# Optimization experiments

Measured on AMD Instinct MI355X. Metric: run time of the kernel, lower is better.

## Reference

```python
import jax, jax.numpy as jnp
import numpy as np

T, B, H = 512, 32, 512   # seq, batch, hidden_dim (hidden has 2*H channels)
D = 512                  # label_dim
V = 32000                # vocab
L = 2048                 # number of labels (spans)
K = 2                    # tags per label (regularized ragged tags)


def setup_inputs() -> dict:
    key = jax.random.key(0)
    ks = jax.random.split(key, 11)
    hidden = jax.random.normal(ks[0], (T, B, 2 * H), dtype=jnp.float32)
    begins = jax.random.randint(ks[1], (L,), 1, T - 1)   # begin-1 >= 0
    ends = jax.random.randint(ks[2], (L,), 1, T - 1)     # end <= T-1, end-1 >= 0
    bids = jax.random.randint(ks[3], (L,), 0, B)
    tags = jax.random.randint(ks[4], (L, K), 0, V)
    s = 1.0 / np.sqrt(2 * H)
    Wc = jax.random.uniform(ks[5], (D, 2 * H), minval=-s, maxval=s, dtype=jnp.float32)
    bc = jax.random.uniform(ks[6], (D,), minval=-s, maxval=s, dtype=jnp.float32)
    Wp = jax.random.uniform(ks[7], (D, 2 * H), minval=-s, maxval=s, dtype=jnp.float32)
    bp = jax.random.uniform(ks[8], (D,), minval=-s, maxval=s, dtype=jnp.float32)
    s2 = 1.0 / np.sqrt(D)
    Wo = jax.random.uniform(ks[9], (V, D), minval=-s2, maxval=s2, dtype=jnp.float32)
    bo = jnp.zeros((V,), jnp.float32)
    # discard probs per SoftmaxLoss._discard_probs from synthetic counts
    counts = jax.random.uniform(ks[10], (V,), minval=0.5, maxval=100.0, dtype=jnp.float32)
    freqs = counts / counts.sum()
    discard_probs = jnp.maximum(1.0 - jnp.sqrt(1e-4 / freqs), 0.0)
    return dict(hidden=hidden, Wc=Wc, bc=bc, Wp=Wp, bp=bp, Wo=Wo, bo=bo,
                discard_probs=discard_probs, begins=begins, ends=ends,
                bids=bids, tags=tags)


def reference(hidden, Wc, bc, Wp, bp, Wo, bo, discard_probs,
              begins, ends, bids, tags):
    Hd = hidden.shape[-1] // 2
    # span gathers (vectorized over all labels)
    h_bm1 = hidden[begins - 1, bids]                 # [L, 2H]
    h_end = hidden[ends, bids]                       # [L, 2H]
    context = jnp.concatenate([h_bm1[:, :Hd], h_end[:, Hd:]], axis=-1)  # [L, 2H]
    phrase = (hidden[begins, bids] + hidden[ends - 1, bids]) * 0.5      # [L, 2H]
    # FFNs (dropout = identity in eval mode)
    cf = jnp.tanh(context @ Wc.T + bc)               # [L, D]
    pf = jnp.tanh(phrase @ Wp.T + bp)                # [L, D]
    feats = jnp.concatenate([cf, pf], axis=0)        # [2L, D]
    # softmax loss with discard-prob scaling
    logsm = jax.nn.log_softmax(feats @ Wo.T + bo, axis=-1)  # [2L, V]
    tg = jnp.concatenate([tags, tags], axis=0)       # [2L, K]
    neg = -jnp.take_along_axis(logsm, tg, axis=-1)   # [2L, K]
    ratio = 1.0 - discard_probs[tg]                  # [2L, K]
    loss_rows = (neg * ratio).sum(-1) / ratio.sum(-1)  # [2L]
    n = tg.shape[0]
    return (loss_rows.sum() / (n + 1e-5)).reshape(1)
```

## Files before the change

### kernel.cpp

```cpp
#include <hip/hip_runtime.h>
#include <stdint.h>

typedef uint16_t u16;
typedef uint8_t  u8;
typedef __bf16 bf16x8 __attribute__((ext_vector_type(8)));
typedef float f32x4 __attribute__((ext_vector_type(4)));
typedef int i32x4 __attribute__((ext_vector_type(4)));
typedef int i32x8 __attribute__((ext_vector_type(8)));

#define NSC    16
#define NTILES 250
#define NPART  (2 * NSC)
#define NROWS  4096

__device__ __forceinline__ u16 f2b(float x) {
    uint32_t u = __float_as_uint(x);
    u += 0x7FFF + ((u >> 16) & 1);
    return (u16)(u >> 16);
}

__device__ __forceinline__ u8 f32_to_fp8(float x) {
    uint32_t sign = (__float_as_uint(x) >> 24) & 0x80;
    float ax = fminf(fabsf(x), 448.f);
    uint32_t r;
    if (ax < 0.015625f) {
        r = (uint32_t)(int)rintf(ax * 512.f);
    } else {
        uint32_t u = __float_as_uint(ax);
        u += 0x0007FFFF + ((u >> 20) & 1);
        r = (((u >> 23) - 120) << 3) | ((u >> 20) & 7);
    }
    return (u8)(sign | r);
}

__device__ __forceinline__ float fp8_val(int b) {
    int e = (b >> 3) & 0xF, m = b & 7;
    float v = e ? __uint_as_float((uint32_t)(((e + 120) << 23) | (m << 20)))
                : (float)m * 0.001953125f;
    return (b & 0x80) ? -v : v;
}

__device__ __forceinline__ void cp16(const void* g, void* l) {
    __builtin_amdgcn_global_load_lds(
        (const __attribute__((address_space(1))) uint32_t*)g,
        (__attribute__((address_space(3))) uint32_t*)l, 16, 0, 0);
}

__device__ __forceinline__ float fast_tanh(float x) {
    x = fminf(15.f, fmaxf(-15.f, x));
    float e = __expf(2.f * x);
    return (e - 1.f) / (e + 1.f);
}

__global__ void k_convert8(const float* __restrict__ src, u8* __restrict__ dst, int n) {
    int i = (blockIdx.x * blockDim.x + threadIdx.x) * 4;
    int stride = gridDim.x * blockDim.x * 4;
    for (; i < n; i += stride) {
        float4 v = *(const float4*)(src + i);
        u8 o[4] = {f32_to_fp8(v.x * 32.f), f32_to_fp8(v.y * 32.f),
                   f32_to_fp8(v.z * 32.f), f32_to_fp8(v.w * 32.f)};
        *(uint32_t*)(dst + i) = *(const uint32_t*)o;
    }
}

__global__ void k_prep(const float* __restrict__ Wc, const float* __restrict__ Wp,
                       const float* __restrict__ hidden, const int* __restrict__ begins,
                       const int* __restrict__ ends, const int* __restrict__ bids,
                       u16* __restrict__ Wc_b, u16* __restrict__ Wp_b,
                       u16* __restrict__ ctx, u16* __restrict__ phr) {
    int b = blockIdx.x;
    if (b < 256) {
        int i = b * 2048 + threadIdx.x * 8;
        float4 a0 = *(const float4*)(Wc + i), a1 = *(const float4*)(Wc + i + 4);
        float4 p0 = *(const float4*)(Wp + i), p1 = *(const float4*)(Wp + i + 4);
        u16 oc[8] = {f2b(a0.x), f2b(a0.y), f2b(a0.z), f2b(a0.w),
                     f2b(a1.x), f2b(a1.y), f2b(a1.z), f2b(a1.w)};
        u16 op[8] = {f2b(p0.x), f2b(p0.y), f2b(p0.z), f2b(p0.w),
                     f2b(p1.x), f2b(p1.y), f2b(p1.z), f2b(p1.w)};
        *(int4*)(Wc_b + i) = *(const int4*)oc;
        *(int4*)(Wp_b + i) = *(const int4*)op;
        return;
    }
    int l = b - 256;
    int bg = begins[l], e = ends[l], bd = bids[l];
    const float* h_bm1 = hidden + ((size_t)(bg - 1) * 32 + bd) * 1024;
    const float* h_e   = hidden + ((size_t)e * 32 + bd) * 1024;
    const float* h_b   = hidden + ((size_t)bg * 32 + bd) * 1024;
    const float* h_em1 = hidden + ((size_t)(e - 1) * 32 + bd) * 1024;
    int d = threadIdx.x * 4;
    float4 c4 = (d < 512) ? *(const float4*)(h_bm1 + d) : *(const float4*)(h_e + d);
    float4 b4 = *(const float4*)(h_b + d);
    float4 e4 = *(const float4*)(h_em1 + d);
    u16 co[4] = {f2b(c4.x), f2b(c4.y), f2b(c4.z), f2b(c4.w)};
    u16 po[4] = {f2b(0.5f * (b4.x + e4.x)), f2b(0.5f * (b4.y + e4.y)),
                 f2b(0.5f * (b4.z + e4.z)), f2b(0.5f * (b4.w + e4.w))};
    *(uint64_t*)(ctx + (size_t)l * 1024 + d) = *(const uint64_t*)co;
    *(uint64_t*)(phr + (size_t)l * 1024 + d) = *(const uint64_t*)po;
}

__global__ __launch_bounds__(256) void k_feats(const u16* __restrict__ ctx, const u16* __restrict__ phr,
        const u16* __restrict__ Wc, const u16* __restrict__ Wp,
        const float* __restrict__ bc, const float* __restrict__ bp,
        u8* __restrict__ feats) {
    __shared__ __align__(16) u16 lA[64 * 32];
    __shared__ __align__(16) u16 lB[64 * 32];
    int z = blockIdx.z;
    const u16* A = z ? phr : ctx;
    const u16* W = z ? Wp : Wc;
    const float* bias = z ? bp : bc;
    int m0 = blockIdx.x * 64;
    int n0 = blockIdx.y * 64;
    int t = threadIdx.x;
    int lane = t & 63, w = t >> 6;
    int lrow = lane & 15, lq = lane >> 4;
    f32x4 zero = {0.f, 0.f, 0.f, 0.f};
    f32x4 acc[4];
    for (int i = 0; i < 4; i++) acc[i] = zero;
    int row = t >> 2, kseg = (t & 3) * 8;
    for (int kt = 0; kt < 32; kt++) {
        int k0 = kt * 32;
        __syncthreads();
        cp16(&A[(size_t)(m0 + row) * 1024 + k0 + kseg], &lA[t * 8]);
        cp16(&W[(size_t)(n0 + row) * 1024 + k0 + kseg], &lB[t * 8]);
        __syncthreads();
        bf16x8 af = *(bf16x8*)&lA[(w * 16 + lrow) * 32 + lq * 8];
        for (int ns = 0; ns < 4; ns++) {
            bf16x8 bfr = *(bf16x8*)&lB[(ns * 16 + lrow) * 32 + lq * 8];
            acc[ns] = __builtin_amdgcn_mfma_f32_16x16x32_bf16(af, bfr, acc[ns], 0, 0, 0);
        }
    }
    int zbase = z * 2048;
    for (int ns = 0; ns < 4; ns++) {
        int col = n0 + ns * 16 + lrow;
        float bv = bias[col];
        for (int r = 0; r < 4; r++) {
            int orow = zbase + m0 + w * 16 + lq * 4 + r;
            feats[(size_t)orow * 512 + col] = f32_to_fp8(16.f * fast_tanh(acc[ns][r] + bv));
        }
    }
}

__global__ __launch_bounds__(256) void k_lse(const u8* __restrict__ feats,
        const u8* __restrict__ Wo, const float* __restrict__ bo, float* __restrict__ ps) {
    __shared__ __align__(16) u8 lds[2][2][128 * 128];
    int m0 = blockIdx.x * 128;
    int sc = blockIdx.y;
    int ts = (NTILES * sc) / NSC, te = (NTILES * (sc + 1)) / NSC;
    int t = threadIdx.x;
    int lane = t & 63, w = t >> 6;
    int lrow = lane & 15, lq = lane >> 4;
    int wrow = (w & 1) * 64, wcol = (w >> 1) * 64;
    int xm = lrow & 7;
    int xoA = ((2 * lq) ^ xm) * 16;
    int xoB = ((2 * lq + 1) ^ xm) * 16;

    int srow = t >> 3;
    int kb = ((t & 7) ^ ((t >> 3) & 7)) * 16;
    const u8* pA = feats + (size_t)(m0 + srow) * 512 + kb;

    int rowA[4], rowB[4];
    for (int i = 0; i < 4; i++) {
        rowA[i] = (wrow + i * 16 + lrow) * 128;
        rowB[i] = (wcol + i * 16 + lrow) * 128;
    }

    float s_state[4][4];
    for (int mi = 0; mi < 4; mi++)
        for (int r = 0; r < 4; r++) s_state[mi][r] = 0.f;
    f32x4 zero = {0.f, 0.f, 0.f, 0.f};
    f32x4 acc[4][4];
    const float inv512 = 1.f / 512.f;

    auto stage = [&](int buf, int gr) {
        int k0 = (gr & 3) * 128;
        const u8* pB = Wo + (size_t)((gr >> 2) * 128 + srow) * 512 + kb;
        const u8* pA2 = pA + k0;
        for (int j = 0; j < 4; j++) {
            cp16(pA2 + (size_t)(32 * j) * 512, &lds[buf][0][t * 16 + j * 4096]);
            cp16(pB + k0 + (size_t)(32 * j) * 512, &lds[buf][1][t * 16 + j * 4096]);
        }
    };

    int gr0 = ts * 4, gr1 = te * 4;
    stage(0, gr0);
    for (int gr = gr0; gr < gr1; gr++) {
        int cur = gr & 1;
        __syncthreads();
        if (gr + 1 < gr1) stage(cur ^ 1, gr + 1);
        if ((gr & 3) == 0)
            for (int mi = 0; mi < 4; mi++)
                for (int ni = 0; ni < 4; ni++) acc[mi][ni] = zero;
        const u8* bufA = lds[cur][0];
        const u8* bufB = lds[cur][1];
        i32x8 af[4];
        for (int mi = 0; mi < 4; mi++) {
            i32x4 lo = *(const i32x4*)(bufA + rowA[mi] + xoA);
            i32x4 hi = *(const i32x4*)(bufA + rowA[mi] + xoB);
            af[mi] = __builtin_shufflevector(lo, hi, 0, 1, 2, 3, 4, 5, 6, 7);
        }
        for (int ni = 0; ni < 4; ni++) {
            i32x4 blo = *(const i32x4*)(bufB + rowB[ni] + xoA);
            i32x4 bhi = *(const i32x4*)(bufB + rowB[ni] + xoB);
            i32x8 bf8 = __builtin_shufflevector(blo, bhi, 0, 1, 2, 3, 4, 5, 6, 7);
            for (int mi = 0; mi < 4; mi++)
                acc[mi][ni] = __builtin_amdgcn_mfma_scale_f32_16x16x128_f8f6f4(
                    af[mi], bf8, acc[mi][ni], 0, 0,
                    0, 0x7F7F7F7F, 0, 0x7F7F7F7F);
        }
        if ((gr & 3) == 3) {
            int n0 = (gr >> 2) * 128;
            for (int ni = 0; ni < 4; ni++) {
                float bv = bo[n0 + wcol + ni * 16 + lrow];
                for (int mi = 0; mi < 4; mi++)
                    for (int r = 0; r < 4; r++)
                        s_state[mi][r] += __expf(fmaf(acc[mi][ni][r], inv512, bv));
            }
        }
    }
    for (int mi = 0; mi < 4; mi++)
    for (int r = 0; r < 4; r++) {
        float s = s_state[mi][r];
        for (int off = 1; off < 16; off <<= 1) s += __shfl_xor(s, off);
        if (lrow == 0) {
            int row = m0 + wrow + mi * 16 + lq * 4 + r;
            ps[row * NPART + sc * 2 + (w >> 1)] = s;
        }
    }
}

__global__ void k_taglog(const u8* __restrict__ feats, const u8* __restrict__ Wo,
        const float* __restrict__ bo, const int* __restrict__ tags, float* __restrict__ tlog) {
    int i = blockIdx.x * 4 + (threadIdx.x >> 6);
    int lane = threadIdx.x & 63;
    int t0 = tags[(i & 2047) * 2 + 0];
    int t1 = tags[(i & 2047) * 2 + 1];
    uint64_t fa = *(const uint64_t*)(feats + (size_t)i * 512 + lane * 8);
    uint64_t wa = *(const uint64_t*)(Wo + (size_t)t0 * 512 + lane * 8);
    uint64_t wb = *(const uint64_t*)(Wo + (size_t)t1 * 512 + lane * 8);
    float s0 = 0.f, s1 = 0.f;
    for (int j = 0; j < 8; j++) {
        float fv = fp8_val((int)((fa >> (8 * j)) & 0xFF));
        s0 += fv * fp8_val((int)((wa >> (8 * j)) & 0xFF));
        s1 += fv * fp8_val((int)((wb >> (8 * j)) & 0xFF));
    }
    for (int off = 32; off >= 1; off >>= 1) {
        s0 += __shfl_down(s0, off);
        s1 += __shfl_down(s1, off);
    }
    if (lane == 0) {
        tlog[i * 2 + 0] = s0 * (1.f / 512.f) + bo[t0];
        tlog[i * 2 + 1] = s1 * (1.f / 512.f) + bo[t1];
    }
}

__global__ void k_final(const float* __restrict__ ps,
        const float* __restrict__ tlog, const int* __restrict__ tags,
        const float* __restrict__ dp, float* __restrict__ out) {
    __shared__ float red[256];
    int i = blockIdx.x * 256 + threadIdx.x;
    float S = 0.f;
    for (int j = 0; j < NPART; j++) S += ps[i * NPART + j];
    float lse = logf(S);
    float num = 0.f, den = 0.f;
    for (int k = 0; k < 2; k++) {
        int tg = tags[(i & 2047) * 2 + k];
        float r = 1.0f - dp[tg];
        num += r * (lse - tlog[i * 2 + k]);
        den += r;
    }
    red[threadIdx.x] = num / den;
    __syncthreads();
    for (int s = 128; s > 0; s >>= 1) {
        if (threadIdx.x < s) red[threadIdx.x] += red[threadIdx.x + s];
        __syncthreads();
    }
    if (threadIdx.x == 0) atomicAdd(out, red[0] / (4096.0f + 1e-5f));
}

extern "C" void kernel_launch(void* const* d_in, const int* in_sizes, int n_in,
                              void* d_out, int out_size, void* d_ws, size_t ws_size,
                              hipStream_t stream) {
    const float* hidden = (const float*)d_in[0];
    const float* Wc     = (const float*)d_in[1];
    const float* bc     = (const float*)d_in[2];
    const float* Wp     = (const float*)d_in[3];
    const float* bp     = (const float*)d_in[4];
    const float* Wo     = (const float*)d_in[5];
    const float* bo     = (const float*)d_in[6];
    const float* dp     = (const float*)d_in[7];
    const int* begins   = (const int*)d_in[8];
    const int* ends     = (const int*)d_in[9];
    const int* bids     = (const int*)d_in[10];
    const int* tags     = (const int*)d_in[11];
    float* out = (float*)d_out;

    u8*  Wo8     = (u8*)d_ws;
    u16* Wc_b    = (u16*)((char*)d_ws + 16384000);
    u16* Wp_b    = Wc_b + 524288;
    u16* ctx_b   = Wp_b + 524288;
    u16* phr_b   = ctx_b + 2097152;
    u8*  feats8  = (u8*)(phr_b + 2097152);
    float* ps    = (float*)ctx_b;
    float* tlog  = ps + NROWS * NPART;

    k_convert8<<<2048, 256, 0, stream>>>(Wo, Wo8, 16384000);
    k_prep<<<2304, 256, 0, stream>>>(Wc, Wp, hidden, begins, ends, bids,
                                     Wc_b, Wp_b, ctx_b, phr_b);
    k_feats<<<dim3(32, 8, 2), 256, 0, stream>>>(ctx_b, phr_b, Wc_b, Wp_b, bc, bp, feats8);
    k_lse<<<dim3(32, NSC), 256, 0, stream>>>(feats8, Wo8, bo, ps);
    k_taglog<<<1024, 256, 0, stream>>>(feats8, Wo8, bo, tags, tlog);
    hipMemsetAsync(d_out, 0, sizeof(float), stream);
    k_final<<<16, 256, 0, stream>>>(ps, tlog, tags, dp, out);
}
```

Measured before the change: 280.0 us.

## Keep A fragments in registers and deepen B staging to four LDS slots

The LSE GEMM kernel now loads the whole 128x512 fp8 A block for each warp into registers once, so only Wo tiles are streamed through LDS. B staging moves from a double buffer to a four-slot ring with three tiles in flight, using explicit vmcnt waits and raw s_barrier in place of __syncthreads. It also raises MFMA issue priority and sets launch bounds for 2 blocks per CU. This halves LDS traffic and deepens prefetch, at the cost of many more VGPRs held for A fragments. It also relies on hand-counted waitcnt values being correct.

```diff
diff --git a/kernel.cpp b/kernel.cpp
--- a/kernel.cpp
+++ b/kernel.cpp
@@ -140,9 +140,9 @@
     }
 }
 
-__global__ __launch_bounds__(256) void k_lse(const u8* __restrict__ feats,
+__global__ __launch_bounds__(256, 2) void k_lse(const u8* __restrict__ feats,
         const u8* __restrict__ Wo, const float* __restrict__ bo, float* __restrict__ ps) {
-    __shared__ __align__(16) u8 lds[2][2][128 * 128];
+    __shared__ __align__(16) u8 lds[4][128 * 128];
     int m0 = blockIdx.x * 128;
     int sc = blockIdx.y;
     int ts = (NTILES * sc) / NSC, te = (NTILES * (sc + 1)) / NSC;
@@ -156,13 +156,24 @@
 
     int srow = t >> 3;
     int kb = ((t & 7) ^ ((t >> 3) & 7)) * 16;
-    const u8* pA = feats + (size_t)(m0 + srow) * 512 + kb;
-
-    int rowA[4], rowB[4];
-    for (int i = 0; i < 4; i++) {
-        rowA[i] = (wrow + i * 16 + lrow) * 128;
-        rowB[i] = (wcol + i * 16 + lrow) * 128;
-    }
+
+    i32x8 af[4][4];
+#pragma unroll
+    for (int mi = 0; mi < 4; mi++)
+#pragma unroll
+        for (int kc = 0; kc < 4; kc++) {
+            const u8* pa = feats + (size_t)(m0 + wrow + mi * 16 + lrow) * 512
+                         + kc * 128 + lq * 32;
+            i32x4 lo = *(const i32x4*)pa;
+            i32x4 hi = *(const i32x4*)(pa + 16);
+            af[mi][kc] = __builtin_shufflevector(lo, hi, 0, 1, 2, 3, 4, 5, 6, 7);
+        }
+
+    auto stageB = [&](int slot, int gr) {
+        const u8* pB = Wo + (size_t)((gr >> 2) * 128 + srow) * 512 + (gr & 3) * 128 + kb;
+        for (int j = 0; j < 4; j++)
+            cp16(pB + (size_t)(32 * j) * 512, &lds[slot][t * 16 + j * 4096]);
+    };
 
     float s_state[4][4];
     for (int mi = 0; mi < 4; mi++)
@@ -171,50 +182,54 @@
     f32x4 acc[4][4];
     const float inv512 = 1.f / 512.f;
 
-    auto stage = [&](int buf, int gr) {
-        int k0 = (gr & 3) * 128;
-        const u8* pB = Wo + (size_t)((gr >> 2) * 128 + srow) * 512 + kb;
-        const u8* pA2 = pA + k0;
-        for (int j = 0; j < 4; j++) {
-            cp16(pA2 + (size_t)(32 * j) * 512, &lds[buf][0][t * 16 + j * 4096]);
-            cp16(pB + k0 + (size_t)(32 * j) * 512, &lds[buf][1][t * 16 + j * 4096]);
-        }
-    };
-
-    int gr0 = ts * 4, gr1 = te * 4;
-    stage(0, gr0);
-    for (int gr = gr0; gr < gr1; gr++) {
-        int cur = gr & 1;
-        __syncthreads();
-        if (gr + 1 < gr1) stage(cur ^ 1, gr + 1);
-        if ((gr & 3) == 0)
+    int gr0 = ts * 4;
+    stageB(0, gr0);
+    stageB(1, gr0 + 1);
+    stageB(2, gr0 + 2);
+
+    for (int tile = ts; tile < te; ++tile) {
+        int grt = tile * 4;
+        bool notlast = (tile + 1 < te);
+#pragma unroll
+        for (int mi = 0; mi < 4; mi++)
+#pragma unroll
+            for (int ni = 0; ni < 4; ni++) acc[mi][ni] = zero;
+#pragma unroll
+        for (int kc = 0; kc < 4; kc++) {
+            if (notlast || kc < 2)
+                asm volatile("s_waitcnt vmcnt(8)" ::: "memory");
+            else if (kc == 2)
+                asm volatile("s_waitcnt vmcnt(4)" ::: "memory");
+            else
+                asm volatile("s_waitcnt vmcnt(0)" ::: "memory");
+            __builtin_amdgcn_s_barrier();
+            if (notlast || kc == 0)
+                stageB((kc + 3) & 3, grt + kc + 3);
+            const u8* bufB = lds[kc];
+            __builtin_amdgcn_s_setprio(1);
+#pragma unroll
+            for (int ni = 0; ni < 4; ni++) {
+                const u8* pb = bufB + (wcol + ni * 16 + lrow) * 128;
+                i32x4 blo = *(const i32x4*)(pb + xoA);
+                i32x4 bhi = *(const i32x4*)(pb + xoB);
+                i32x8 bfr = __builtin_shufflevector(blo, bhi, 0, 1, 2, 3, 4, 5, 6, 7);
+#pragma unroll
+                for (int mi = 0; mi < 4; mi++)
+                    acc[mi][ni] = __builtin_amdgcn_mfma_scale_f32_16x16x128_f8f6f4(
+                        af[mi][kc], bfr, acc[mi][ni], 0, 0,
+                        0, 0x7F7F7F7F, 0, 0x7F7F7F7F);
+            }
+            __builtin_amdgcn_s_setprio(0);
+        }
+        int n0 = tile * 128;
+#pragma unroll
+        for (int ni = 0; ni < 4; ni++) {
+            float bv = bo[n0 + wcol + ni * 16 + lrow];
+#pragma unroll
             for (int mi = 0; mi < 4; mi++)
-                for (int ni = 0; ni < 4; ni++) acc[mi][ni] = zero;
-        const u8* bufA = lds[cur][0];
-        const u8* bufB = lds[cur][1];
-        i32x8 af[4];
-        for (int mi = 0; mi < 4; mi++) {
-            i32x4 lo = *(const i32x4*)(bufA + rowA[mi] + xoA);
-            i32x4 hi = *(const i32x4*)(bufA + rowA[mi] + xoB);
-            af[mi] = __builtin_shufflevector(lo, hi, 0, 1, 2, 3, 4, 5, 6, 7);
-        }
-        for (int ni = 0; ni < 4; ni++) {
-            i32x4 blo = *(const i32x4*)(bufB + rowB[ni] + xoA);
-            i32x4 bhi = *(const i32x4*)(bufB + rowB[ni] + xoB);
-            i32x8 bf8 = __builtin_shufflevector(blo, bhi, 0, 1, 2, 3, 4, 5, 6, 7);
-            for (int mi = 0; mi < 4; mi++)
-                acc[mi][ni] = __builtin_amdgcn_mfma_scale_f32_16x16x128_f8f6f4(
-                    af[mi], bf8, acc[mi][ni], 0, 0,
-                    0, 0x7F7F7F7F, 0, 0x7F7F7F7F);
-        }
-        if ((gr & 3) == 3) {
-            int n0 = (gr >> 2) * 128;
-            for (int ni = 0; ni < 4; ni++) {
-                float bv = bo[n0 + wcol + ni * 16 + lrow];
-                for (int mi = 0; mi < 4; mi++)
-                    for (int r = 0; r < 4; r++)
-                        s_state[mi][r] += __expf(fmaf(acc[mi][ni][r], inv512, bv));
-            }
+#pragma unroll
+                for (int r = 0; r < 4; r++)
+                    s_state[mi][r] += __expf(fmaf(acc[mi][ni][r], inv512, bv));
         }
     }
     for (int mi = 0; mi < 4; mi++)
```

Result: no change. 279.0 us (-0.4%).
